# Optimization experiments

Hardware: AMD Instinct MI355X
Metric: run time of the kernel (lower is better)

Reference implementation:

```python
import jax, jax.numpy as jnp
import numpy as np
import math

DROPOUT_P = 0.1

def setup_inputs() -> dict:
    key = jax.random.key(0)
    kq, kk, kv = jax.random.split(key, 3)
    B, S, H, D = 2, 2048, 16, 64
    return {
        "query": jax.random.normal(kq, (B, S, H, D), dtype=jnp.float32),
        "key": jax.random.normal(kk, (B, S, H, D), dtype=jnp.float32),
        "value": jax.random.normal(kv, (B, S, H, D), dtype=jnp.float32),
    }

def reference(query, key, value):
    # [B,S,H,D] -> [B,H,S,D]
    q = jnp.transpose(query, (0, 2, 1, 3))
    k = jnp.transpose(key, (0, 2, 1, 3))
    v = jnp.transpose(value, (0, 2, 1, 3))
    scale = 1.0 / math.sqrt(q.shape[-1])
    # scores: [B,H,S,S] in fp32 (matches div.to(float32))
    div = jnp.einsum('bhqd,bhkd->bhqk', q, k).astype(jnp.float32) * scale
    attn = jax.nn.softmax(div, axis=-1)
    # dropout (training=True), deterministic fixed key
    keep = jax.random.bernoulli(jax.random.key(42), 1.0 - DROPOUT_P, attn.shape)
    attn = jnp.where(keep, attn / (1.0 - DROPOUT_P), 0.0)
    attn = attn.astype(jnp.float16)
    # fp16 weights @ fp32 values (promotes to fp32 in jax)
    out = jnp.einsum('bhqk,bhkd->bhqd', attn, v)
    return out
```

## Files before the change

### kernel.cpp

```cpp
#include <hip/hip_runtime.h>

#define BB 2
#define HH 16
#define SS 2048
#define DD 64
#define QT 64
#define KT 64
#define LP 72

using bf16x8 = __attribute__((ext_vector_type(8))) short;
using half8  = __attribute__((ext_vector_type(8))) _Float16;
using f32x4  = __attribute__((ext_vector_type(4))) float;

__device__ __forceinline__ unsigned tf_bits(unsigned i) {
  const unsigned ks1 = 42u;
  const unsigned ks2 = 0x1BD11BDAu ^ 42u;
  unsigned x0 = 0u;
  unsigned x1 = i + ks1;
#define TF_R(r) { x0 += x1; x1 = __builtin_rotateleft32(x1, r) ^ x0; }
  TF_R(13) TF_R(15) TF_R(26) TF_R(6)
  x0 += ks1; x1 += ks2 + 1u;
  TF_R(17) TF_R(29) TF_R(16) TF_R(24)
  x0 += ks2; x1 += 2u;
  TF_R(13) TF_R(15) TF_R(26) TF_R(6)
   x1 += ks1 + 3u;
  TF_R(17) TF_R(29) TF_R(16) TF_R(24)
  x0 += ks1; x1 += ks2 + 4u;
  TF_R(13) TF_R(15) TF_R(26) TF_R(6)
  x0 += ks2; x1 += 5u;
#undef TF_R
  return x0 ^ x1;
}

__global__ __launch_bounds__(256, 4)
void fused_attn_mfma(const float* __restrict__ Qg, const float* __restrict__ Kg,
                     const float* __restrict__ Vg, float* __restrict__ Og) {
  __shared__ __attribute__((aligned(16))) unsigned short Ks_hi[KT][LP];
  __shared__ __attribute__((aligned(16))) unsigned short Ks_lo[KT][LP];
  __shared__ __attribute__((aligned(16))) _Float16 Vt[DD][LP];
  __shared__ __attribute__((aligned(16))) _Float16 Ps[QT][LP];

  const int t   = threadIdx.x;
  const int w   = t >> 6;
  const int l   = t & 63;
  const int l15 = l & 15;
  const int hi4 = l >> 4;

  const int qt0 = blockIdx.x * QT;
  const int bh  = blockIdx.y;
  const int b   = bh >> 4, h = bh & 15;

  auto gidx = [&](int s) { return (((size_t)b * SS + s) * HH + h) * DD; };

  bf16x8 qh[2], ql[2];
  {
    const float* qp = Qg + gidx(qt0 + 16 * w + l15) + hi4 * 8;
    #pragma unroll
    for (int c = 0; c < 2; ++c) {
      float f[8];
      *(float4*)&f[0] = *(const float4*)(qp + c * 32);
      *(float4*)&f[4] = *(const float4*)(qp + c * 32 + 4);
      #pragma unroll
      for (int j = 0; j < 8; ++j) {
        float qs = 0.125f * f[j];
        unsigned u = __float_as_uint(qs);
        qh[c][j] = (short)(u >> 16);
        float lo = qs - __uint_as_float(u & 0xFFFF0000u);
        ql[c][j] = (short)(__float_as_uint(lo) >> 16);
      }
    }
  }

  f32x4 o[4];
  #pragma unroll
  for (int i = 0; i < 4; ++i) o[i] = (f32x4){0.f, 0.f, 0.f, 0.f};
  float mrow = -1e30f, lrow = 0.f;

  const unsigned fb =
      ((unsigned)bh * SS + (unsigned)(qt0 + 16 * w + l15)) * SS + (unsigned)(hi4 * 4);

  const int rK = t >> 2, cK = (t & 3) * 16;
  const int rV = t & 63, cV = (t >> 6) * 16;
  const float* kp = Kg + gidx(rK) + cK;
  const float* vp = Vg + gidx(rV) + cV;
  const size_t kstride = (size_t)KT * HH * DD;

  #pragma unroll 1
  for (int kt = 0; kt < SS / KT; ++kt, kp += kstride, vp += kstride) {
    __syncthreads();

    {
      unsigned short khs[16], kls[16];
      #pragma unroll
      for (int u4 = 0; u4 < 4; ++u4) {
        float4 kv = *(const float4*)(kp + u4 * 4);
        float ff[4] = {kv.x, kv.y, kv.z, kv.w};
        #pragma unroll
        for (int j = 0; j < 4; ++j) {
          unsigned u = __float_as_uint(ff[j]);
          khs[u4 * 4 + j] = (unsigned short)(u >> 16);
          float lo = ff[j] - __uint_as_float(u & 0xFFFF0000u);
          kls[u4 * 4 + j] = (unsigned short)(__float_as_uint(lo) >> 16);
        }
      }
      *(bf16x8*)&Ks_hi[rK][cK]     = *(bf16x8*)&khs[0];
      *(bf16x8*)&Ks_hi[rK][cK + 8] = *(bf16x8*)&khs[8];
      *(bf16x8*)&Ks_lo[rK][cK]     = *(bf16x8*)&kls[0];
      *(bf16x8*)&Ks_lo[rK][cK + 8] = *(bf16x8*)&kls[8];
    }
    {
      #pragma unroll
      for (int u4 = 0; u4 < 4; ++u4) {
        float4 vv = *(const float4*)(vp + u4 * 4);
        float ff[4] = {vv.x, vv.y, vv.z, vv.w};
        #pragma unroll
        for (int j = 0; j < 4; ++j)
          Vt[cV + u4 * 4 + j][rV] = (_Float16)ff[j];
      }
    }
    __syncthreads();

    f32x4 s4[4];
    #pragma unroll
    for (int k4 = 0; k4 < 4; ++k4) {
      f32x4 a = (f32x4){0.f, 0.f, 0.f, 0.f};
      #pragma unroll
      for (int c = 0; c < 2; ++c) {
        bf16x8 kh = *(const bf16x8*)&Ks_hi[k4 * 16 + l15][c * 32 + hi4 * 8];
        bf16x8 kl = *(const bf16x8*)&Ks_lo[k4 * 16 + l15][c * 32 + hi4 * 8];
        a = __builtin_amdgcn_mfma_f32_16x16x32_bf16(kh, qh[c], a, 0, 0, 0);
        a = __builtin_amdgcn_mfma_f32_16x16x32_bf16(kh, ql[c], a, 0, 0, 0);
        a = __builtin_amdgcn_mfma_f32_16x16x32_bf16(kl, qh[c], a, 0, 0, 0);
      }
      s4[k4] = a;
    }

    unsigned bts[16];
    {
      const unsigned ib = fb + (unsigned)(kt * KT);
      #pragma unroll
      for (int k4 = 0; k4 < 4; ++k4)
        #pragma unroll
        for (int r = 0; r < 4; ++r)
          bts[k4 * 4 + r] = tf_bits(ib + (unsigned)(k4 * 16 + r));
    }

    float mx01 = fmaxf(fmaxf(s4[0][0], s4[0][1]), fmaxf(s4[0][2], s4[0][3]));
    float mx23 = fmaxf(fmaxf(s4[1][0], s4[1][1]), fmaxf(s4[1][2], s4[1][3]));
    float mx45 = fmaxf(fmaxf(s4[2][0], s4[2][1]), fmaxf(s4[2][2], s4[2][3]));
    float mx67 = fmaxf(fmaxf(s4[3][0], s4[3][1]), fmaxf(s4[3][2], s4[3][3]));
    float mx = fmaxf(fmaxf(mx01, mx23), fmaxf(mx45, mx67));
    mx = fmaxf(mx, __shfl_xor(mx, 16, 64));
    mx = fmaxf(mx, __shfl_xor(mx, 32, 64));
    const float mn = fmaxf(mrow, mx);
    const bool grew = !__all(mn == mrow);
    const float rr = __expf(mrow - mn);
    #pragma unroll
    for (int k4 = 0; k4 < 4; ++k4) {
      s4[k4][0] = __expf(s4[k4][0] - mn);
      s4[k4][1] = __expf(s4[k4][1] - mn);
      s4[k4][2] = __expf(s4[k4][2] - mn);
      s4[k4][3] = __expf(s4[k4][3] - mn);
    }
    float ps0 = (s4[0][0] + s4[0][1]) + (s4[0][2] + s4[0][3]);
    float ps1 = (s4[1][0] + s4[1][1]) + (s4[1][2] + s4[1][3]);
    float ps2 = (s4[2][0] + s4[2][1]) + (s4[2][2] + s4[2][3]);
    float ps3 = (s4[3][0] + s4[3][1]) + (s4[3][2] + s4[3][3]);
    float ps = (ps0 + ps1) + (ps2 + ps3);
    ps += __shfl_xor(ps, 16, 64);
    ps += __shfl_xor(ps, 32, 64);
    lrow = lrow * rr + ps;
    mrow = mn;

    #pragma unroll
    for (int k4 = 0; k4 < 4; ++k4) {
      union { uint2 u2; _Float16 hh[4]; } pk;
      #pragma unroll
      for (int r = 0; r < 4; ++r) {
        float pv = (bts[k4 * 4 + r] < 0xE6666600u) ? s4[k4][r] : 0.f;
        pk.hh[r] = (_Float16)pv;
      }
      *(uint2*)&Ps[16 * w + l15][k4 * 16 + hi4 * 4] = pk.u2;
    }
    __syncthreads();

    half8 pa[2];
    #pragma unroll
    for (int c = 0; c < 2; ++c)
      pa[c] = *(const half8*)&Ps[16 * w + l15][c * 32 + hi4 * 8];
    if (grew) {
      float rfs[4];
      #pragma unroll
      for (int r = 0; r < 4; ++r) rfs[r] = __shfl(rr, hi4 * 4 + r, 64);
      #pragma unroll
      for (int dt = 0; dt < 4; ++dt)
        #pragma unroll
        for (int i = 0; i < 4; ++i) o[dt][i] *= rfs[i];
    }
    #pragma unroll
    for (int dt = 0; dt < 4; ++dt) {
      f32x4 a = o[dt];
      #pragma unroll
      for (int c = 0; c < 2; ++c) {
        half8 vh = *(const half8*)&Vt[dt * 16 + l15][c * 32 + hi4 * 8];
        a = __builtin_amdgcn_mfma_f32_16x16x32_f16(pa[c], vh, a, 0, 0, 0);
      }
      o[dt] = a;
    }
  }

  float lr[4];
  #pragma unroll
  for (int r = 0; r < 4; ++r) lr[r] = __shfl(lrow, hi4 * 4 + r, 64);
  #pragma unroll
  for (int r4 = 0; r4 < 4; ++r4) {
    const float inv = 1.0f / (lr[r4] * 0.9f);
    const size_t ob = ((size_t)bh * SS + (qt0 + 16 * w + hi4 * 4 + r4)) * DD + l15;
    #pragma unroll
    for (int dt = 0; dt < 4; ++dt)
      Og[ob + dt * 16] = o[dt][r4] * inv;
  }
}

extern "C" void kernel_launch(void* const* d_in, const int* in_sizes, int n_in,
                              void* d_out, int out_size, void* d_ws, size_t ws_size,
                              hipStream_t stream) {
  const float* Q = (const float*)d_in[0];
  const float* K = (const float*)d_in[1];
  const float* V = (const float*)d_in[2];
  float* O = (float*)d_out;
  dim3 grid(SS / QT, BB * HH);
  fused_attn_mfma<<<grid, dim3(256), 0, stream>>>(Q, K, V, O);
}
```

Before: 327.1 us.

## Pre-convert K/V into swizzled workspace tiles and stream via global_load_lds

Adds a prep kernel that splits K into bf16 hi/lo and transposes V to fp16 once per call. It writes them into XOR-swizzled 8KB tiles in the workspace. The main kernel then fills LDS with direct global-to-LDS loads instead of converting K/V in every query block. This removes redundant conversion work and transposed LDS stores, at the cost of an extra launch and workspace traffic. It also drops the barrier between writing Ps and reading it back, which relies on each wave only reading its own rows.

```diff
diff --git a/kernel.cpp b/kernel.cpp
--- a/kernel.cpp
+++ b/kernel.cpp
@@ -6,11 +6,22 @@
 #define DD 64
 #define QT 64
 #define KT 64
+#define NKT (SS / KT)
 #define LP 72
+#define TILE_BYTES 8192
+#define WS_KHI 0
+#define WS_KLO (32u * 32u * 8192u)
+#define WS_VT  (2u * 32u * 32u * 8192u)
+#define WS_NEED ((size_t)3 * 32 * 32 * 8192)
 
 using bf16x8 = __attribute__((ext_vector_type(8))) short;
 using half8  = __attribute__((ext_vector_type(8))) _Float16;
 using f32x4  = __attribute__((ext_vector_type(4))) float;
+
+typedef __attribute__((address_space(3))) unsigned lds_u32;
+typedef __attribute__((address_space(1))) unsigned gvm_u32;
+#define GLOAD16(gp, lp) \
+  __builtin_amdgcn_global_load_lds((gvm_u32*)(gp), (lds_u32*)(lp), 16, 0, 0)
 
 __device__ __forceinline__ unsigned tf_bits(unsigned i) {
   const unsigned ks1 = 42u;
@@ -23,7 +34,7 @@
   TF_R(17) TF_R(29) TF_R(16) TF_R(24)
   x0 += ks2; x1 += 2u;
   TF_R(13) TF_R(15) TF_R(26) TF_R(6)
-   x1 += ks1 + 3u;
+  x1 += ks1 + 3u;
   TF_R(17) TF_R(29) TF_R(16) TF_R(24)
   x0 += ks1; x1 += ks2 + 4u;
   TF_R(13) TF_R(15) TF_R(26) TF_R(6)
@@ -32,12 +43,50 @@
   return x0 ^ x1;
 }
 
+__global__ __launch_bounds__(256)
+void prep_kv(const float* __restrict__ Kg, const float* __restrict__ Vg,
+             char* __restrict__ ws) {
+  const int g = blockIdx.x * 256 + threadIdx.x;
+  if (blockIdx.x < 2048) {
+    const int ck = g & 7, row = (g >> 3) & 63, kt = (g >> 9) & 31, bh = g >> 14;
+    const int b = bh >> 4, h = bh & 15;
+    const float* src = Kg + (((size_t)b * SS + kt * 64 + row) * HH + h) * DD + ck * 8;
+    float f[8];
+    *(float4*)&f[0] = ((const float4*)src)[0];
+    *(float4*)&f[4] = ((const float4*)src)[1];
+    unsigned short hi[8], lo[8];
+    #pragma unroll
+    for (int j = 0; j < 8; ++j) {
+      unsigned u = __float_as_uint(f[j]);
+      hi[j] = (unsigned short)(u >> 16);
+      float l = f[j] - __uint_as_float(u & 0xFFFF0000u);
+      lo[j] = (unsigned short)(__float_as_uint(l) >> 16);
+    }
+    const size_t toff = (size_t)(bh * NKT + kt) * TILE_BYTES + row * 128 +
+                        ((unsigned)(ck ^ (row & 7))) * 16;
+    *(uint4*)(ws + WS_KHI + toff) = *(uint4*)hi;
+    *(uint4*)(ws + WS_KLO + toff) = *(uint4*)lo;
+  } else {
+    const int g2 = g - (1 << 19);
+    const int d = g2 & 63, ck = (g2 >> 6) & 7, kt = (g2 >> 9) & 31, bh = g2 >> 14;
+    const int b = bh >> 4, h = bh & 15;
+    const float* src = Vg + (((size_t)b * SS + kt * 64 + ck * 8) * HH + h) * DD + d;
+    _Float16 hv[8];
+    #pragma unroll
+    for (int j = 0; j < 8; ++j)
+      hv[j] = (_Float16)src[(size_t)j * HH * DD];
+    const size_t toff = (size_t)(bh * NKT + kt) * TILE_BYTES + d * 128 +
+                        ((unsigned)(ck ^ (d & 7))) * 16;
+    *(uint4*)(ws + WS_VT + toff) = *(uint4*)hv;
+  }
+}
+
 __global__ __launch_bounds__(256, 4)
-void fused_attn_mfma(const float* __restrict__ Qg, const float* __restrict__ Kg,
-                     const float* __restrict__ Vg, float* __restrict__ Og) {
-  __shared__ __attribute__((aligned(16))) unsigned short Ks_hi[KT][LP];
-  __shared__ __attribute__((aligned(16))) unsigned short Ks_lo[KT][LP];
-  __shared__ __attribute__((aligned(16))) _Float16 Vt[DD][LP];
+void fused_attn_ws(const float* __restrict__ Qg, const char* __restrict__ ws,
+                   float* __restrict__ Og) {
+  __shared__ __attribute__((aligned(16))) unsigned short KsHi[4096];
+  __shared__ __attribute__((aligned(16))) unsigned short KsLo[4096];
+  __shared__ __attribute__((aligned(16))) _Float16 VtL[4096];
   __shared__ __attribute__((aligned(16))) _Float16 Ps[QT][LP];
 
   const int t   = threadIdx.x;
@@ -45,16 +94,15 @@
   const int l   = t & 63;
   const int l15 = l & 15;
   const int hi4 = l >> 4;
+  const int e8  = l15 & 7;
 
   const int qt0 = blockIdx.x * QT;
   const int bh  = blockIdx.y;
   const int b   = bh >> 4, h = bh & 15;
 
-  auto gidx = [&](int s) { return (((size_t)b * SS + s) * HH + h) * DD; };
-
   bf16x8 qh[2], ql[2];
   {
-    const float* qp = Qg + gidx(qt0 + 16 * w + l15) + hi4 * 8;
+    const float* qp = Qg + (((size_t)b * SS + qt0 + 16 * w + l15) * HH + h) * DD + hi4 * 8;
     #pragma unroll
     for (int c = 0; c < 2; ++c) {
       float f[8];
@@ -79,45 +127,22 @@
   const unsigned fb =
       ((unsigned)bh * SS + (unsigned)(qt0 + 16 * w + l15)) * SS + (unsigned)(hi4 * 4);
 
-  const int rK = t >> 2, cK = (t & 3) * 16;
-  const int rV = t & 63, cV = (t >> 6) * 16;
-  const float* kp = Kg + gidx(rK) + cK;
-  const float* vp = Vg + gidx(rV) + cV;
-  const size_t kstride = (size_t)KT * HH * DD;
+  const size_t tbase = (size_t)(bh * NKT) * TILE_BYTES + 2048 * w + 16 * l;
+  const char* khi_p = ws + WS_KHI + tbase;
+  const char* klo_p = ws + WS_KLO + tbase;
+  const char* vt_p  = ws + WS_VT  + tbase;
 
   #pragma unroll 1
-  for (int kt = 0; kt < SS / KT; ++kt, kp += kstride, vp += kstride) {
+  for (int kt = 0; kt < NKT; ++kt,
+       khi_p += TILE_BYTES, klo_p += TILE_BYTES, vt_p += TILE_BYTES) {
     __syncthreads();
 
-    {
-      unsigned short khs[16], kls[16];
-      #pragma unroll
-      for (int u4 = 0; u4 < 4; ++u4) {
-        float4 kv = *(const float4*)(kp + u4 * 4);
-        float ff[4] = {kv.x, kv.y, kv.z, kv.w};
-        #pragma unroll
-        for (int j = 0; j < 4; ++j) {
-          unsigned u = __float_as_uint(ff[j]);
-          khs[u4 * 4 + j] = (unsigned short)(u >> 16);
-          float lo = ff[j] - __uint_as_float(u & 0xFFFF0000u);
-          kls[u4 * 4 + j] = (unsigned short)(__float_as_uint(lo) >> 16);
-        }
-      }
-      *(bf16x8*)&Ks_hi[rK][cK]     = *(bf16x8*)&khs[0];
-      *(bf16x8*)&Ks_hi[rK][cK + 8] = *(bf16x8*)&khs[8];
-      *(bf16x8*)&Ks_lo[rK][cK]     = *(bf16x8*)&kls[0];
-      *(bf16x8*)&Ks_lo[rK][cK + 8] = *(bf16x8*)&kls[8];
-    }
-    {
-      #pragma unroll
-      for (int u4 = 0; u4 < 4; ++u4) {
-        float4 vv = *(const float4*)(vp + u4 * 4);
-        float ff[4] = {vv.x, vv.y, vv.z, vv.w};
-        #pragma unroll
-        for (int j = 0; j < 4; ++j)
-          Vt[cV + u4 * 4 + j][rV] = (_Float16)ff[j];
-      }
-    }
+    GLOAD16(khi_p,        &KsHi[1024 * w]);
+    GLOAD16(khi_p + 1024, &KsHi[1024 * w + 512]);
+    GLOAD16(klo_p,        &KsLo[1024 * w]);
+    GLOAD16(klo_p + 1024, &KsLo[1024 * w + 512]);
+    GLOAD16(vt_p,         &VtL[1024 * w]);
+    GLOAD16(vt_p + 1024,  &VtL[1024 * w + 512]);
     __syncthreads();
 
     f32x4 s4[4];
@@ -126,8 +151,9 @@
       f32x4 a = (f32x4){0.f, 0.f, 0.f, 0.f};
       #pragma unroll
       for (int c = 0; c < 2; ++c) {
-        bf16x8 kh = *(const bf16x8*)&Ks_hi[k4 * 16 + l15][c * 32 + hi4 * 8];
-        bf16x8 kl = *(const bf16x8*)&Ks_lo[k4 * 16 + l15][c * 32 + hi4 * 8];
+        const int co = ((((c << 2) + hi4) ^ e8) << 3);
+        bf16x8 kh = *(const bf16x8*)&KsHi[(k4 * 16 + l15) * 64 + co];
+        bf16x8 kl = *(const bf16x8*)&KsLo[(k4 * 16 + l15) * 64 + co];
         a = __builtin_amdgcn_mfma_f32_16x16x32_bf16(kh, qh[c], a, 0, 0, 0);
         a = __builtin_amdgcn_mfma_f32_16x16x32_bf16(kh, ql[c], a, 0, 0, 0);
         a = __builtin_amdgcn_mfma_f32_16x16x32_bf16(kl, qh[c], a, 0, 0, 0);
@@ -182,7 +208,6 @@
       }
       *(uint2*)&Ps[16 * w + l15][k4 * 16 + hi4 * 4] = pk.u2;
     }
-    __syncthreads();
 
     half8 pa[2];
     #pragma unroll
@@ -202,13 +227,187 @@
       f32x4 a = o[dt];
       #pragma unroll
       for (int c = 0; c < 2; ++c) {
+        const int co = ((((c << 2) + hi4) ^ e8) << 3);
+        half8 vh = *(const half8*)&VtL[(dt * 16 + l15) * 64 + co];
+        a = __builtin_amdgcn_mfma_f32_16x16x32_f16(pa[c], vh, a, 0, 0, 0);
+      }
+      o[dt] = a;
+    }
+  }
+
+  float lr[4];
+  #pragma unroll
+  for (int r = 0; r < 4; ++r) lr[r] = __shfl(lrow, hi4 * 4 + r, 64);
+  #pragma unroll
+  for (int r4 = 0; r4 < 4; ++r4) {
+    const float inv = 1.0f / (lr[r4] * 0.9f);
+    const size_t ob = ((size_t)bh * SS + (qt0 + 16 * w + hi4 * 4 + r4)) * DD + l15;
+    #pragma unroll
+    for (int dt = 0; dt < 4; ++dt)
+      Og[ob + dt * 16] = o[dt][r4] * inv;
+  }
+}
+
+__global__ __launch_bounds__(256, 4)
+void fused_attn_fallback(const float* __restrict__ Qg, const float* __restrict__ Kg,
+                         const float* __restrict__ Vg, float* __restrict__ Og) {
+  __shared__ __attribute__((aligned(16))) unsigned short Ks_hi[KT][LP];
+  __shared__ __attribute__((aligned(16))) unsigned short Ks_lo[KT][LP];
+  __shared__ __attribute__((aligned(16))) _Float16 Vt[DD][LP];
+  __shared__ __attribute__((aligned(16))) _Float16 Ps[QT][LP];
+
+  const int t = threadIdx.x, w = t >> 6, l = t & 63, l15 = l & 15, hi4 = l >> 4;
+  const int qt0 = blockIdx.x * QT, bh = blockIdx.y, b = bh >> 4, h = bh & 15;
+  auto gidx = [&](int s) { return (((size_t)b * SS + s) * HH + h) * DD; };
+
+  bf16x8 qh[2], ql[2];
+  {
+    const float* qp = Qg + gidx(qt0 + 16 * w + l15) + hi4 * 8;
+    #pragma unroll
+    for (int c = 0; c < 2; ++c) {
+      float f[8];
+      *(float4*)&f[0] = *(const float4*)(qp + c * 32);
+      *(float4*)&f[4] = *(const float4*)(qp + c * 32 + 4);
+      #pragma unroll
+      for (int j = 0; j < 8; ++j) {
+        float qs = 0.125f * f[j];
+        unsigned u = __float_as_uint(qs);
+        qh[c][j] = (short)(u >> 16);
+        float lo = qs - __uint_as_float(u & 0xFFFF0000u);
+        ql[c][j] = (short)(__float_as_uint(lo) >> 16);
+      }
+    }
+  }
+  f32x4 o[4];
+  #pragma unroll
+  for (int i = 0; i < 4; ++i) o[i] = (f32x4){0.f, 0.f, 0.f, 0.f};
+  float mrow = -1e30f, lrow = 0.f;
+  const unsigned fb =
+      ((unsigned)bh * SS + (unsigned)(qt0 + 16 * w + l15)) * SS + (unsigned)(hi4 * 4);
+  const int rK = t >> 2, cK = (t & 3) * 16;
+  const int rV = t & 63, cV = (t >> 6) * 16;
+  const float* kp = Kg + gidx(rK) + cK;
+  const float* vp = Vg + gidx(rV) + cV;
+  const size_t kstride = (size_t)KT * HH * DD;
+
+  #pragma unroll 1
+  for (int kt = 0; kt < SS / KT; ++kt, kp += kstride, vp += kstride) {
+    __syncthreads();
+    {
+      unsigned short khs[16], kls[16];
+      #pragma unroll
+      for (int u4 = 0; u4 < 4; ++u4) {
+        float4 kv = *(const float4*)(kp + u4 * 4);
+        float ff[4] = {kv.x, kv.y, kv.z, kv.w};
+        #pragma unroll
+        for (int j = 0; j < 4; ++j) {
+          unsigned u = __float_as_uint(ff[j]);
+          khs[u4 * 4 + j] = (unsigned short)(u >> 16);
+          float lo = ff[j] - __uint_as_float(u & 0xFFFF0000u);
+          kls[u4 * 4 + j] = (unsigned short)(__float_as_uint(lo) >> 16);
+        }
+      }
+      *(bf16x8*)&Ks_hi[rK][cK]     = *(bf16x8*)&khs[0];
+      *(bf16x8*)&Ks_hi[rK][cK + 8] = *(bf16x8*)&khs[8];
+      *(bf16x8*)&Ks_lo[rK][cK]     = *(bf16x8*)&kls[0];
+      *(bf16x8*)&Ks_lo[rK][cK + 8] = *(bf16x8*)&kls[8];
+    }
+    {
+      #pragma unroll
+      for (int u4 = 0; u4 < 4; ++u4) {
+        float4 vv = *(const float4*)(vp + u4 * 4);
+        float ff[4] = {vv.x, vv.y, vv.z, vv.w};
+        #pragma unroll
+        for (int j = 0; j < 4; ++j)
+          Vt[cV + u4 * 4 + j][rV] = (_Float16)ff[j];
+      }
+    }
+    __syncthreads();
+
+    f32x4 s4[4];
+    #pragma unroll
+    for (int k4 = 0; k4 < 4; ++k4) {
+      f32x4 a = (f32x4){0.f, 0.f, 0.f, 0.f};
+      #pragma unroll
+      for (int c = 0; c < 2; ++c) {
+        bf16x8 kh = *(const bf16x8*)&Ks_hi[k4 * 16 + l15][c * 32 + hi4 * 8];
+        bf16x8 kl = *(const bf16x8*)&Ks_lo[k4 * 16 + l15][c * 32 + hi4 * 8];
+        a = __builtin_amdgcn_mfma_f32_16x16x32_bf16(kh, qh[c], a, 0, 0, 0);
+        a = __builtin_amdgcn_mfma_f32_16x16x32_bf16(kh, ql[c], a, 0, 0, 0);
+        a = __builtin_amdgcn_mfma_f32_16x16x32_bf16(kl, qh[c], a, 0, 0, 0);
+      }
+      s4[k4] = a;
+    }
+    unsigned bts[16];
+    {
+      const unsigned ib = fb + (unsigned)(kt * KT);
+      #pragma unroll
+      for (int k4 = 0; k4 < 4; ++k4)
+        #pragma unroll
+        for (int r = 0; r < 4; ++r)
+          bts[k4 * 4 + r] = tf_bits(ib + (unsigned)(k4 * 16 + r));
+    }
+    float mx01 = fmaxf(fmaxf(s4[0][0], s4[0][1]), fmaxf(s4[0][2], s4[0][3]));
+    float mx23 = fmaxf(fmaxf(s4[1][0], s4[1][1]), fmaxf(s4[1][2], s4[1][3]));
+    float mx45 = fmaxf(fmaxf(s4[2][0], s4[2][1]), fmaxf(s4[2][2], s4[2][3]));
+    float mx67 = fmaxf(fmaxf(s4[3][0], s4[3][1]), fmaxf(s4[3][2], s4[3][3]));
+    float mx = fmaxf(fmaxf(mx01, mx23), fmaxf(mx45, mx67));
+    mx = fmaxf(mx, __shfl_xor(mx, 16, 64));
+    mx = fmaxf(mx, __shfl_xor(mx, 32, 64));
+    const float mn = fmaxf(mrow, mx);
+    const bool grew = !__all(mn == mrow);
+    const float rr = __expf(mrow - mn);
+    #pragma unroll
+    for (int k4 = 0; k4 < 4; ++k4) {
+      s4[k4][0] = __expf(s4[k4][0] - mn);
+      s4[k4][1] = __expf(s4[k4][1] - mn);
+      s4[k4][2] = __expf(s4[k4][2] - mn);
+      s4[k4][3] = __expf(s4[k4][3] - mn);
+    }
+    float ps0 = (s4[0][0] + s4[0][1]) + (s4[0][2] + s4[0][3]);
+    float ps1 = (s4[1][0] + s4[1][1]) + (s4[1][2] + s4[1][3]);
+    float ps2 = (s4[2][0] + s4[2][1]) + (s4[2][2] + s4[2][3]);
+    float ps3 = (s4[3][0] + s4[3][1]) + (s4[3][2] + s4[3][3]);
+    float ps = (ps0 + ps1) + (ps2 + ps3);
+    ps += __shfl_xor(ps, 16, 64);
+    ps += __shfl_xor(ps, 32, 64);
+    lrow = lrow * rr + ps;
+    mrow = mn;
+    #pragma unroll
+    for (int k4 = 0; k4 < 4; ++k4) {
+      union { uint2 u2; _Float16 hh[4]; } pk;
+      #pragma unroll
+      for (int r = 0; r < 4; ++r) {
+        float pv = (bts[k4 * 4 + r] < 0xE6666600u) ? s4[k4][r] : 0.f;
+        pk.hh[r] = (_Float16)pv;
+      }
+      *(uint2*)&Ps[16 * w + l15][k4 * 16 + hi4 * 4] = pk.u2;
+    }
+    __syncthreads();
+    half8 pa[2];
+    #pragma unroll
+    for (int c = 0; c < 2; ++c)
+      pa[c] = *(const half8*)&Ps[16 * w + l15][c * 32 + hi4 * 8];
+    if (grew) {
+      float rfs[4];
+      #pragma unroll
+      for (int r = 0; r < 4; ++r) rfs[r] = __shfl(rr, hi4 * 4 + r, 64);
+      #pragma unroll
+      for (int dt = 0; dt < 4; ++dt)
+        #pragma unroll
+        for (int i = 0; i < 4; ++i) o[dt][i] *= rfs[i];
+    }
+    #pragma unroll
+    for (int dt = 0; dt < 4; ++dt) {
+      f32x4 a = o[dt];
+      #pragma unroll
+      for (int c = 0; c < 2; ++c) {
         half8 vh = *(const half8*)&Vt[dt * 16 + l15][c * 32 + hi4 * 8];
         a = __builtin_amdgcn_mfma_f32_16x16x32_f16(pa[c], vh, a, 0, 0, 0);
       }
       o[dt] = a;
     }
   }
-
   float lr[4];
   #pragma unroll
   for (int r = 0; r < 4; ++r) lr[r] = __shfl(lrow, hi4 * 4 + r, 64);
@@ -230,5 +429,11 @@
   const float* V = (const float*)d_in[2];
   float* O = (float*)d_out;
   dim3 grid(SS / QT, BB * HH);
-  fused_attn_mfma<<<grid, dim3(256), 0, stream>>>(Q, K, V, O);
+  if (ws_size >= WS_NEED) {
+    char* wsp = (char*)d_ws;
+    prep_kv<<<4096, 256, 0, stream>>>(K, V, wsp);
+    fused_attn_ws<<<grid, dim3(256), 0, stream>>>(Q, wsp, O);
+  } else {
+    fused_attn_fallback<<<grid, dim3(256), 0, stream>>>(Q, K, V, O);
+  }
 }
```

Result: faster. 311.8 us (-4.7%).
